# Optimization experiments

Measured on AMD Instinct MI355X. Metric: run time of the kernel, lower is better.

Reference implementation:

```python
import jax, jax.numpy as jnp
import numpy as np

SPATIAL_DECAY = 50.0
POS_SCALE = 1000.0  # spread positions so decay=50 gives realistic locality


def setup_inputs() -> dict:
    key = jax.random.key(0)
    k1, k2 = jax.random.split(key)
    N, D = 8192, 512
    features = jax.random.normal(k1, (N, D), dtype=jnp.float32)
    positions = jax.random.uniform(k2, (N, 2), dtype=jnp.float32) * POS_SCALE
    lambda_weight = jnp.asarray(0.5, dtype=jnp.float32)  # nn.Parameter init
    temperature = jnp.asarray(1.0, dtype=jnp.float32)    # nn.Parameter init
    return {"features": features, "positions": positions,
            "lambda_weight": lambda_weight, "temperature": temperature, "k": 20}


def reference(features, positions, lambda_weight, temperature, k):
    N = features.shape[0]
    # F.normalize(dim=1), eps=1e-12
    norms = jnp.linalg.norm(features, axis=1, keepdims=True)
    feat_norm = features / jnp.maximum(norms, 1e-12)
    sim = feat_norm @ feat_norm.T                                   # (N, N)
    # squared euclidean distances (cdist(p=2) then **2 == squared dist)
    sq = jnp.sum(positions * positions, axis=1)                      # (N,)
    d2 = jnp.maximum(sq[:, None] + sq[None, :] - 2.0 * (positions @ positions.T), 0.0)
    spatial = jnp.exp(-d2 / (2.0 * SPATIAL_DECAY ** 2))             # (N, N)
    lam = jax.nn.sigmoid(lambda_weight)
    adj = jax.nn.sigmoid((lam * sim + (1.0 - lam) * spatial) * temperature)
    # row-wise top-k mask, scatter 1.0 at top-k columns
    _, topk_idx = jax.lax.top_k(adj, k)                              # (N, k)
    rows = jnp.arange(N)[:, None]
    mask = jnp.zeros_like(adj).at[rows, topk_idx].set(1.0)
    return adj * mask, lam
```

## Files before the change

### kernel.cpp

```cpp
#include <hip/hip_runtime.h>
#include <hip/hip_fp16.h>
#include <math.h>

#define N 8192
#define D 512
#define KSEL 20
#define CAND_CAP 256
#define WINDOW 2.5e-3f
#define BS_EXTRA 6.2e-4f
#define ROWU 8192
#define FS_A 4096

typedef __attribute__((ext_vector_type(8))) short short8;
typedef __attribute__((ext_vector_type(4))) float f32x4;

__device__ __forceinline__ unsigned short f2bf(float x) {
  unsigned int u = __float_as_uint(x);
  unsigned int r = u + 0x7FFFu + ((u >> 16) & 1u);
  return (unsigned short)(r >> 16);
}

__device__ __forceinline__ unsigned int packh2(float a, float b) {
  return (unsigned int)__half_as_ushort(__float2half(a)) |
         ((unsigned int)__half_as_ushort(__float2half(b)) << 16);
}

__device__ __forceinline__ void gld16(const unsigned short* g, unsigned short* l) {
  __builtin_amdgcn_global_load_lds(
      (const __attribute__((address_space(1))) unsigned int*)g,
      (__attribute__((address_space(3))) unsigned int*)l, 16, 0, 0);
}

__device__ __forceinline__ int swz(int row, int cp) {
  return row * 64 + ((((cp >> 2) ^ (row & 15)) << 2) | (cp & 3));
}
__device__ __forceinline__ int swz4(int row, int q) {
  return row * 64 + ((q ^ (row & 15)) << 2);
}

__global__ __launch_bounds__(256) void prep_kernel(
    const float* __restrict__ feat, const float* __restrict__ pos,
    const float* __restrict__ lamw,
    float* __restrict__ normf, float* __restrict__ sqf,
    float* __restrict__ fn32, unsigned short* __restrict__ fnbf,
    float* __restrict__ out) {
  __shared__ float rowbuf[4][512];
  int w = threadIdx.x >> 6, lane = threadIdx.x & 63;
  float* rb = rowbuf[w];
  for (int i = 0; i < 8; i++) {
    int row = blockIdx.x * 32 + w * 8 + i;
    const float* f = feat + (size_t)row * D;
    float4 v0 = *(const float4*)(f + 4 * lane);
    float4 v1 = *(const float4*)(f + 256 + 4 * lane);
    *(float4*)&rb[4 * lane] = v0;
    *(float4*)&rb[256 + 4 * lane] = v1;
    __builtin_amdgcn_s_waitcnt(0);
    float s = 0.f;
    if (lane < 32) {
      int b = lane >> 3, j = lane & 7;
      const float* a = rb + b * 128 + j;
      float r = __fmul_rn(a[0], a[0]);
      #pragma unroll
      for (int k = 1; k < 16; k++)
        r = __fadd_rn(r, __fmul_rn(a[8 * k], a[8 * k]));
      r = __fadd_rn(r, __shfl_xor(r, 1, 64));
      r = __fadd_rn(r, __shfl_xor(r, 2, 64));
      r = __fadd_rn(r, __shfl_xor(r, 4, 64));
      r = __fadd_rn(r, __shfl_xor(r, 8, 64));
      r = __fadd_rn(r, __shfl_xor(r, 16, 64));
      s = r;
    }
    float st = __shfl(s, 0, 64);
    float nrm = fmaxf(__fsqrt_rn(st), 1e-12f);
    if (lane == 0) {
      normf[row] = nrm;
      float x = pos[2 * row], y = pos[2 * row + 1];
      sqf[row] = __fadd_rn(__fmul_rn(x, x), __fmul_rn(y, y));
      if (row == 0) {
        float e = (float)exp(-(double)lamw[0]);
        out[(size_t)N * N] = 1.0f / __fadd_rn(1.0f, e);
      }
    }
    float4 q0, q1;
    q0.x = v0.x / nrm; q0.y = v0.y / nrm; q0.z = v0.z / nrm; q0.w = v0.w / nrm;
    q1.x = v1.x / nrm; q1.y = v1.y / nrm; q1.z = v1.z / nrm; q1.w = v1.w / nrm;
    *(float4*)(fn32 + (size_t)row * D + 4 * lane) = q0;
    *(float4*)(fn32 + (size_t)row * D + 256 + 4 * lane) = q1;
    uint2 o0, o1;
    o0.x = (unsigned int)f2bf(q0.x) | ((unsigned int)f2bf(q0.y) << 16);
    o0.y = (unsigned int)f2bf(q0.z) | ((unsigned int)f2bf(q0.w) << 16);
    o1.x = (unsigned int)f2bf(q1.x) | ((unsigned int)f2bf(q1.y) << 16);
    o1.y = (unsigned int)f2bf(q1.z) | ((unsigned int)f2bf(q1.w) << 16);
    *(uint2*)(fnbf + (size_t)row * D + 4 * lane) = o0;
    *(uint2*)(fnbf + (size_t)row * D + 256 + 4 * lane) = o1;
  }
}

__global__ __launch_bounds__(256) void adj_kernel(
    const unsigned short* __restrict__ G,
    const float* __restrict__ pos, const float* __restrict__ sqf,
    const float* __restrict__ lamw, const float* __restrict__ temp,
    unsigned int* __restrict__ filt, int fs,
    unsigned int* __restrict__ out_u, int mode) {
  __shared__ __align__(16) unsigned char smem[32768];
  unsigned short* As = (unsigned short*)smem;
  unsigned short* Bs = As + 8192;
  unsigned int* tileT = (unsigned int*)smem;

  int L = blockIdx.x;
  int tid = threadIdx.x;

  if (L < 2048) {
    uint4 z = {0u, 0u, 0u, 0u};
    if (mode == 0) {
      size_t base = (size_t)L * 32768;
      #pragma unroll
      for (int it = 0; it < 32; it++)
        *(uint4*)(out_u + base + it * 1024 + tid * 4) = z;
    } else {
      #pragma unroll
      for (int it = 0; it < 16; it++) {
        int g = L * 16384 + it * 1024 + tid * 4;
        int r = g >> 12, c = g & 4095;
        *(uint4*)(out_u + (size_t)r * ROWU + 4096 + c) = z;
      }
    }
  }

  int by = (int)((129.0 - sqrt(129.0 * 129.0 - 8.0 * (double)L)) * 0.5);
  while (64 * (by + 1) - ((by + 1) * by) / 2 <= L) by++;
  while (64 * by - (by * (by - 1)) / 2 > L) by--;
  int bx = by + (L - (64 * by - (by * (by - 1)) / 2));

  int wave = tid >> 6, lane = tid & 63;
  int wr = (wave >> 1) * 64, wc = (wave & 1) * 64;
  int m = lane & 15, quad = lane >> 4;

  f32x4 acc[4][4];
  #pragma unroll
  for (int i = 0; i < 4; i++)
    #pragma unroll
    for (int j = 0; j < 4; j++) acc[i][j] = (f32x4){0.f, 0.f, 0.f, 0.f};

  for (int kt = 0; kt < D / 64; kt++) {
    #pragma unroll
    for (int i = 0; i < 4; i++) {
      int f = i * 256 + tid;
      int r = f >> 3, c = f & 7;
      int cs = (c + r) & 7;
      size_t goff = (size_t)r * D + kt * 64 + cs * 8;
      gld16(G + (size_t)(by * 128) * D + goff, &As[f * 8]);
      gld16(G + (size_t)(bx * 128) * D + goff, &Bs[f * 8]);
    }
    __syncthreads();
    #pragma unroll
    for (int h = 0; h < 2; h++) {
      short8 fa[4], fb[4];
      #pragma unroll
      for (int ti = 0; ti < 4; ti++) {
        int row = wr + ti * 16 + m;
        int cc = ((h * 4 + quad) - row) & 7;
        fa[ti] = *(const short8*)&As[row * 64 + cc * 8];
      }
      #pragma unroll
      for (int tj = 0; tj < 4; tj++) {
        int row = wc + tj * 16 + m;
        int cc = ((h * 4 + quad) - row) & 7;
        fb[tj] = *(const short8*)&Bs[row * 64 + cc * 8];
      }
      #pragma unroll
      for (int ti = 0; ti < 4; ti++)
        #pragma unroll
        for (int tj = 0; tj < 4; tj++)
          acc[ti][tj] = __builtin_amdgcn_mfma_f32_16x16x32_bf16(
              fa[ti], fb[tj], acc[ti][tj], 0, 0, 0);
    }
    __syncthreads();
  }

  float lam = 1.f / (1.f + __expf(-lamw[0]));
  float T = temp[0];
  float oml = 1.f - lam;
  bool offdiag = (bx != by);

  #pragma unroll
  for (int ti = 0; ti < 4; ti++) {
    int gi0 = by * 128 + wr + ti * 16 + quad * 4;
    float xi[4], yi[4], sqi[4];
    #pragma unroll
    for (int r = 0; r < 4; r++) {
      int gi = gi0 + r;
      xi[r] = pos[2 * gi]; yi[r] = pos[2 * gi + 1]; sqi[r] = sqf[gi];
    }
    #pragma unroll
    for (int tj = 0; tj < 4; tj++) {
      int gj = bx * 128 + wc + tj * 16 + m;
      float xj = pos[2 * gj], yj = pos[2 * gj + 1], sj = sqf[gj];
      f32x4 c = acc[ti][tj];
      float sv[4];
      #pragma unroll
      for (int r = 0; r < 4; r++) {
        float d2 = fmaxf(sqi[r] + sj - 2.f * (xi[r] * xj + yi[r] * yj), 0.f);
        float sp = __expf(-d2 * (1.f / 5000.f));
        sv[r] = (lam * c[r] + oml * sp) * T;
      }
      int cpL = (wc + tj * 16 + m) >> 1;
      #pragma unroll
      for (int r = 0; r < 4; r++) {
        float pv = __shfl_xor(sv[r], 1, 64);
        if (!(lane & 1)) {
          int rowL = wr + ti * 16 + quad * 4 + r;
          tileT[swz(rowL, cpL)] = packh2(sv[r], pv);
        }
      }
    }
  }
  __syncthreads();

  #pragma unroll
  for (int it = 0; it < 8; it++) {
    int idx4 = it * 256 + tid;
    int row = idx4 >> 4, q = idx4 & 15;
    uint4 v = *(uint4*)&tileT[swz4(row, q)];
    *(uint4*)(filt + (size_t)(by * 128 + row) * fs + bx * 64 + q * 4) = v;
  }

  if (offdiag) {
    #pragma unroll
    for (int it = 0; it < 8; it++) {
      int idx4 = it * 256 + tid;
      int c = idx4 >> 4, q = idx4 & 15;
      unsigned int wv[4];
      #pragma unroll
      for (int d = 0; d < 4; d++) {
        int p = q * 4 + d;
        unsigned int lo = tileT[swz(2 * p, c >> 1)];
        unsigned int hi = tileT[swz(2 * p + 1, c >> 1)];
        unsigned int h0 = (c & 1) ? (lo >> 16) : (lo & 0xFFFFu);
        unsigned int h1 = (c & 1) ? (hi >> 16) : (hi & 0xFFFFu);
        wv[d] = h0 | (h1 << 16);
      }
      uint4 v; v.x = wv[0]; v.y = wv[1]; v.z = wv[2]; v.w = wv[3];
      *(uint4*)(filt + (size_t)(bx * 128 + c) * fs + by * 64 + q * 4) = v;
    }
  }
}

__global__ __launch_bounds__(256, 4) void topk_kernel(
    const float* __restrict__ pos, const float* __restrict__ sqf,
    const float* __restrict__ lamw, const float* __restrict__ temp,
    const float* __restrict__ fn32,
    const unsigned int* __restrict__ filt, int fs,
    float* __restrict__ out, int doZero) {
  __shared__ float ai[D];
  __shared__ int   redi[2][4];
  __shared__ int   candIdx[CAND_CAP];
  __shared__ float candV[CAND_CAP];
  __shared__ int   selIdx[KSEL];
  __shared__ float selVal[KSEL];
  __shared__ int   cnt;

  int row = blockIdx.x, t = threadIdx.x;
  int lane = t & 63, wid = t >> 6;
  float* orow = out + (size_t)row * N;
  const uint4* fu4 = (const uint4*)(filt + (size_t)row * fs);
  const float* fn_i = fn32 + (size_t)row * D;

  float rv[32];
  #pragma unroll
  for (int q = 0; q < 4; q++) {
    uint4 u = fu4[t + 256 * q];
    unsigned int w[4] = {u.x, u.y, u.z, u.w};
    #pragma unroll
    for (int d = 0; d < 4; d++) {
      __half2 h2 = *reinterpret_cast<__half2*>(&w[d]);
      rv[8 * q + 2 * d]     = __low2float(h2);
      rv[8 * q + 2 * d + 1] = __high2float(h2);
    }
  }
  for (int k = t; k < D; k += 256) ai[k] = fn_i[k];
  if (t == 0) cnt = 0;
  __syncthreads();

  if (doZero) {
    float4 z4 = {0.f, 0.f, 0.f, 0.f};
    #pragma unroll
    for (int i = 0; i < 4; i++) *(float4*)&orow[4 * t + 1024 * i] = z4;
  }

  float lo = -1.0f, hi = 1.5f;
  for (int it = 0; it < 12; it++) {
    float mid = 0.5f * (lo + hi);
    int c = 0;
    #pragma unroll
    for (int q = 0; q < 32; q++) c += (rv[q] >= mid) ? 1 : 0;
    #pragma unroll
    for (int off = 32; off > 0; off >>= 1) c += __shfl_down(c, off, 64);
    if (lane == 0) redi[it & 1][wid] = c;
    __syncthreads();
    int tot = redi[it & 1][0] + redi[it & 1][1] + redi[it & 1][2] + redi[it & 1][3];
    if (tot >= KSEL) lo = mid; else hi = mid;
  }

  float thr = lo - (WINDOW + BS_EXTRA);
  #pragma unroll
  for (int q = 0; q < 32; q++) {
    if (rv[q] >= thr) {
      int p = atomicAdd(&cnt, 1);
      if (p < CAND_CAP) candIdx[p] = 8 * (t + 256 * (q >> 3)) + (q & 7);
    }
  }
  __syncthreads();
  int ncand = min(cnt, CAND_CAP);

  float lamf;
  { float e = (float)exp(-(double)lamw[0]); lamf = 1.0f / __fadd_rn(1.0f, e); }
  float omlf = __fadd_rn(1.0f, -lamf);
  float Tf = temp[0];
  float sq_i = sqf[row];
  float xi = pos[2 * row], yi = pos[2 * row + 1];

  if (t < ncand) {
    int j = candIdx[t];
    const float* fj = fn32 + (size_t)j * D;
    float accv = 0.0f;
    float4 buf[4], nxt[4];
    #pragma unroll
    for (int q = 0; q < 4; q++) buf[q] = *(const float4*)(fj + q * 4);
    for (int c16 = 0; c16 < 32; c16++) {
      if (c16 < 31) {
        #pragma unroll
        for (int q = 0; q < 4; q++)
          nxt[q] = *(const float4*)(fj + (c16 + 1) * 16 + q * 4);
      }
      #pragma unroll
      for (int q = 0; q < 4; q++) {
        float4 a4 = *(const float4*)&ai[c16 * 16 + q * 4];
        accv = __fmaf_rn(a4.x, buf[q].x, accv);
        accv = __fmaf_rn(a4.y, buf[q].y, accv);
        accv = __fmaf_rn(a4.z, buf[q].z, accv);
        accv = __fmaf_rn(a4.w, buf[q].w, accv);
      }
      #pragma unroll
      for (int q = 0; q < 4; q++) buf[q] = nxt[q];
    }
    float xj = pos[2 * j], yj = pos[2 * j + 1];
    float dot2 = __fmaf_rn(yi, yj, __fmul_rn(xi, xj));
    float Ssum = __fadd_rn(sq_i, sqf[j]);
    float d2 = fmaxf(__fadd_rn(Ssum, -__fmul_rn(2.0f, dot2)), 0.0f);
    float arg = (-d2) / 5000.0f;
    float sp = (float)exp((double)arg);
    float u = __fmul_rn(__fadd_rn(__fmul_rn(lamf, accv), __fmul_rn(omlf, sp)), Tf);
    float e = (float)exp(-(double)u);
    candV[t] = 1.0f / __fadd_rn(1.0f, e);
  }
  __syncthreads();

  if (t < 64) {
    for (int s = 0; s < KSEL; s++) {
      float bu = -1.0f; int bj = N, bs = 0;
      for (int c = t; c < ncand; c += 64) {
        float v = candV[c]; int j = candIdx[c];
        if (v > bu || (v == bu && j < bj)) { bu = v; bj = j; bs = c; }
      }
      #pragma unroll
      for (int off = 32; off > 0; off >>= 1) {
        float ov = __shfl_down(bu, off, 64);
        int   oj = __shfl_down(bj, off, 64);
        int   os = __shfl_down(bs, off, 64);
        if (ov > bu || (ov == bu && oj < bj)) { bu = ov; bj = oj; bs = os; }
      }
      if (t == 0) { selIdx[s] = bj; selVal[s] = bu; candV[bs] = -1.0f; }
      __builtin_amdgcn_s_waitcnt(0);
    }
  }
  __syncthreads();
  if (t < KSEL) orow[selIdx[t]] = selVal[t];
}

extern "C" void kernel_launch(void* const* d_in, const int* in_sizes, int n_in,
                              void* d_out, int out_size, void* d_ws, size_t ws_size,
                              hipStream_t stream) {
  const float* feat = (const float*)d_in[0];
  const float* pos  = (const float*)d_in[1];
  const float* lamw = (const float*)d_in[2];
  const float* temp = (const float*)d_in[3];
  float* out = (float*)d_out;
  unsigned int* out_u = (unsigned int*)d_out;

  float* normf = (float*)d_ws;
  float* sqf   = normf + N;
  float* fn32  = sqf + N;
  unsigned short* fnbf = (unsigned short*)(fn32 + (size_t)N * D);
  unsigned int* filtA = (unsigned int*)(fnbf + (size_t)N * D);
  size_t needA = (size_t)2 * N * 4 + (size_t)N * D * 4 + (size_t)N * D * 2 +
                 (size_t)N * FS_A * 4;

  prep_kernel<<<N / 32, 256, 0, stream>>>(feat, pos, lamw, normf, sqf,
                                          fn32, fnbf, out);
  if (ws_size >= needA) {
    adj_kernel<<<2080, 256, 0, stream>>>(fnbf, pos, sqf, lamw, temp,
                                         filtA, FS_A, out_u, 0);
    topk_kernel<<<N, 256, 0, stream>>>(pos, sqf, lamw, temp, fn32,
                                       filtA, FS_A, out, 0);
  } else {
    adj_kernel<<<2080, 256, 0, stream>>>(fnbf, pos, sqf, lamw, temp,
                                         out_u, ROWU, out_u, 1);
    topk_kernel<<<N, 256, 0, stream>>>(pos, sqf, lamw, temp, fn32,
                                       out_u, ROWU, out, 1);
  }
}
```

Measured before the change: 570.8 us.

## Process one row per wavefront in topk kernel with packed half2 threshold search

```diff
diff --git a/kernel.cpp b/kernel.cpp
--- a/kernel.cpp
+++ b/kernel.cpp
@@ -5,9 +5,7 @@
 #define N 8192
 #define D 512
 #define KSEL 20
-#define CAND_CAP 256
-#define WINDOW 2.5e-3f
-#define BS_EXTRA 6.2e-4f
+#define CAND_CAP 320
 #define ROWU 8192
 #define FS_A 4096
 
@@ -246,72 +244,88 @@
   }
 }
 
-__global__ __launch_bounds__(256, 4) void topk_kernel(
+__global__ __launch_bounds__(256) void topk_kernel(
     const float* __restrict__ pos, const float* __restrict__ sqf,
     const float* __restrict__ lamw, const float* __restrict__ temp,
     const float* __restrict__ fn32,
     const unsigned int* __restrict__ filt, int fs,
     float* __restrict__ out, int doZero) {
-  __shared__ float ai[D];
-  __shared__ int   redi[2][4];
-  __shared__ int   candIdx[CAND_CAP];
-  __shared__ float candV[CAND_CAP];
-  __shared__ int   selIdx[KSEL];
-  __shared__ float selVal[KSEL];
-  __shared__ int   cnt;
-
-  int row = blockIdx.x, t = threadIdx.x;
-  int lane = t & 63, wid = t >> 6;
+  __shared__ float ai[4][D];
+  __shared__ int   candIdx[4][CAND_CAP];
+  __shared__ float candV[4][CAND_CAP];
+  __shared__ int   selIdx[4][KSEL];
+  __shared__ float selVal[4][KSEL];
+  __shared__ int   cnt[4];
+
+  int w = threadIdx.x >> 6, lane = threadIdx.x & 63;
+  int row = blockIdx.x * 4 + w;
   float* orow = out + (size_t)row * N;
   const uint4* fu4 = (const uint4*)(filt + (size_t)row * fs);
   const float* fn_i = fn32 + (size_t)row * D;
 
-  float rv[32];
-  #pragma unroll
-  for (int q = 0; q < 4; q++) {
-    uint4 u = fu4[t + 256 * q];
-    unsigned int w[4] = {u.x, u.y, u.z, u.w};
-    #pragma unroll
-    for (int d = 0; d < 4; d++) {
-      __half2 h2 = *reinterpret_cast<__half2*>(&w[d]);
-      rv[8 * q + 2 * d]     = __low2float(h2);
-      rv[8 * q + 2 * d + 1] = __high2float(h2);
-    }
-  }
-  for (int k = t; k < D; k += 256) ai[k] = fn_i[k];
-  if (t == 0) cnt = 0;
-  __syncthreads();
-
-  if (doZero) {
-    float4 z4 = {0.f, 0.f, 0.f, 0.f};
-    #pragma unroll
-    for (int i = 0; i < 4; i++) *(float4*)&orow[4 * t + 1024 * i] = z4;
+  if (lane == 0) cnt[w] = 0;
+
+  unsigned int rv[64];
+  #pragma unroll
+  for (int q = 0; q < 16; q++) {
+    uint4 u = fu4[lane + 64 * q];
+    rv[4 * q] = u.x; rv[4 * q + 1] = u.y; rv[4 * q + 2] = u.z; rv[4 * q + 3] = u.w;
+  }
+  {
+    float4 a0 = *(const float4*)(fn_i + 4 * lane);
+    float4 a1 = *(const float4*)(fn_i + 256 + 4 * lane);
+    *(float4*)&ai[w][4 * lane] = a0;
+    *(float4*)&ai[w][256 + 4 * lane] = a1;
   }
 
   float lo = -1.0f, hi = 1.5f;
   for (int it = 0; it < 12; it++) {
     float mid = 0.5f * (lo + hi);
-    int c = 0;
-    #pragma unroll
-    for (int q = 0; q < 32; q++) c += (rv[q] >= mid) ? 1 : 0;
-    #pragma unroll
-    for (int off = 32; off > 0; off >>= 1) c += __shfl_down(c, off, 64);
-    if (lane == 0) redi[it & 1][wid] = c;
-    __syncthreads();
-    int tot = redi[it & 1][0] + redi[it & 1][1] + redi[it & 1][2] + redi[it & 1][3];
-    if (tot >= KSEL) lo = mid; else hi = mid;
-  }
-
-  float thr = lo - (WINDOW + BS_EXTRA);
-  #pragma unroll
-  for (int q = 0; q < 32; q++) {
-    if (rv[q] >= thr) {
-      int p = atomicAdd(&cnt, 1);
-      if (p < CAND_CAP) candIdx[p] = 8 * (t + 256 * (q >> 3)) + (q & 7);
-    }
-  }
-  __syncthreads();
-  int ncand = min(cnt, CAND_CAP);
+    __half2 m2 = __float2half2_rn(mid);
+    __half2 a2 = __float2half2_rn(0.f);
+    #pragma unroll
+    for (int r = 0; r < 64; r++) {
+      __half2 hv = *(__half2*)&rv[r];
+      a2 = __hadd2(a2, __hge2(hv, m2));
+    }
+    int c = (int)(__low2float(a2) + __high2float(a2));
+    #pragma unroll
+    for (int off = 32; off > 0; off >>= 1) c += __shfl_xor(c, off, 64);
+    if (c >= KSEL) lo = mid; else hi = mid;
+  }
+
+  float thr = lo - 3.7e-3f;
+  __half2 t2 = __float2half2_rn(thr - 6e-4f);
+  int myhits = 0;
+  #pragma unroll
+  for (int r = 0; r < 64; r++) {
+    __half2 hv = *(__half2*)&rv[r];
+    __half2 ge = __hge2(hv, t2);
+    unsigned int g = *(unsigned int*)&ge;
+    if (g) {
+      int j0 = 8 * lane + 512 * (r >> 2) + 2 * (r & 3);
+      if (g & 0xFFFFu) {
+        int p = atomicAdd(&cnt[w], 1);
+        if (p < CAND_CAP) candIdx[w][p] = j0;
+        myhits++;
+      }
+      if (g >> 16) {
+        int p = atomicAdd(&cnt[w], 1);
+        if (p < CAND_CAP) candIdx[w][p] = j0 + 1;
+        myhits++;
+      }
+    }
+  }
+  #pragma unroll
+  for (int off = 32; off > 0; off >>= 1) myhits += __shfl_xor(myhits, off, 64);
+  int ncand = min(myhits, CAND_CAP);
+  __builtin_amdgcn_s_waitcnt(0);
+
+  if (doZero) {
+    float4 z4 = {0.f, 0.f, 0.f, 0.f};
+    #pragma unroll
+    for (int i = 0; i < 16; i++) *(float4*)&orow[4 * lane + 256 * i] = z4;
+  }
 
   float lamf;
   { float e = (float)exp(-(double)lamw[0]); lamf = 1.0f / __fadd_rn(1.0f, e); }
@@ -320,8 +334,8 @@
   float sq_i = sqf[row];
   float xi = pos[2 * row], yi = pos[2 * row + 1];
 
-  if (t < ncand) {
-    int j = candIdx[t];
+  for (int ci = lane; ci < ncand; ci += 64) {
+    int j = candIdx[w][ci];
     const float* fj = fn32 + (size_t)j * D;
     float accv = 0.0f;
     float4 buf[4], nxt[4];
@@ -335,7 +349,7 @@
       }
       #pragma unroll
       for (int q = 0; q < 4; q++) {
-        float4 a4 = *(const float4*)&ai[c16 * 16 + q * 4];
+        float4 a4 = *(const float4*)&ai[w][c16 * 16 + q * 4];
         accv = __fmaf_rn(a4.x, buf[q].x, accv);
         accv = __fmaf_rn(a4.y, buf[q].y, accv);
         accv = __fmaf_rn(a4.z, buf[q].z, accv);
@@ -352,30 +366,29 @@
     float sp = (float)exp((double)arg);
     float u = __fmul_rn(__fadd_rn(__fmul_rn(lamf, accv), __fmul_rn(omlf, sp)), Tf);
     float e = (float)exp(-(double)u);
-    candV[t] = 1.0f / __fadd_rn(1.0f, e);
-  }
-  __syncthreads();
-
-  if (t < 64) {
-    for (int s = 0; s < KSEL; s++) {
-      float bu = -1.0f; int bj = N, bs = 0;
-      for (int c = t; c < ncand; c += 64) {
-        float v = candV[c]; int j = candIdx[c];
-        if (v > bu || (v == bu && j < bj)) { bu = v; bj = j; bs = c; }
-      }
-      #pragma unroll
-      for (int off = 32; off > 0; off >>= 1) {
-        float ov = __shfl_down(bu, off, 64);
-        int   oj = __shfl_down(bj, off, 64);
-        int   os = __shfl_down(bs, off, 64);
-        if (ov > bu || (ov == bu && oj < bj)) { bu = ov; bj = oj; bs = os; }
-      }
-      if (t == 0) { selIdx[s] = bj; selVal[s] = bu; candV[bs] = -1.0f; }
-      __builtin_amdgcn_s_waitcnt(0);
-    }
-  }
-  __syncthreads();
-  if (t < KSEL) orow[selIdx[t]] = selVal[t];
+    candV[w][ci] = 1.0f / __fadd_rn(1.0f, e);
+  }
+  __builtin_amdgcn_s_waitcnt(0);
+
+  for (int s = 0; s < KSEL; s++) {
+    float bu = -1.0f; int bj = N, bs = 0;
+    for (int c = lane; c < ncand; c += 64) {
+      float v = candV[w][c]; int j = candIdx[w][c];
+      if (v > bu || (v == bu && j < bj)) { bu = v; bj = j; bs = c; }
+    }
+    #pragma unroll
+    for (int off = 32; off > 0; off >>= 1) {
+      float ov = __shfl_down(bu, off, 64);
+      int   oj = __shfl_down(bj, off, 64);
+      int   os = __shfl_down(bs, off, 64);
+      if (ov > bu || (ov == bu && oj < bj)) { bu = ov; bj = oj; bs = os; }
+    }
+    if (lane == 0) { selIdx[w][s] = bj; selVal[w][s] = bu; candV[w][bs] = -1.0f; }
+    __builtin_amdgcn_s_waitcnt(0);
+  }
+
+  __builtin_amdgcn_s_waitcnt(0);
+  if (lane < KSEL) orow[selIdx[w][lane]] = selVal[w][lane];
 }
 
 extern "C" void kernel_launch(void* const* d_in, const int* in_sizes, int n_in,
@@ -401,12 +414,12 @@
   if (ws_size >= needA) {
     adj_kernel<<<2080, 256, 0, stream>>>(fnbf, pos, sqf, lamw, temp,
                                          filtA, FS_A, out_u, 0);
-    topk_kernel<<<N, 256, 0, stream>>>(pos, sqf, lamw, temp, fn32,
-                                       filtA, FS_A, out, 0);
+    topk_kernel<<<N / 4, 256, 0, stream>>>(pos, sqf, lamw, temp, fn32,
+                                           filtA, FS_A, out, 0);
   } else {
     adj_kernel<<<2080, 256, 0, stream>>>(fnbf, pos, sqf, lamw, temp,
                                          out_u, ROWU, out_u, 1);
-    topk_kernel<<<N, 256, 0, stream>>>(pos, sqf, lamw, temp, fn32,
-                                       out_u, ROWU, out, 1);
-  }
-}
+    topk_kernel<<<N / 4, 256, 0, stream>>>(pos, sqf, lamw, temp, fn32,
+                                           out_u, ROWU, out, 1);
+  }
+}
```

Result: slower. 853.0 us (+49.4%).

## Interleave output zeroing with GEMM loads and use packed half2 threshold counting

Applied to the files above, without the earlier changes.

```diff
diff --git a/kernel.cpp b/kernel.cpp
--- a/kernel.cpp
+++ b/kernel.cpp
@@ -5,9 +5,7 @@
 #define N 8192
 #define D 512
 #define KSEL 20
-#define CAND_CAP 256
-#define WINDOW 2.5e-3f
-#define BS_EXTRA 6.2e-4f
+#define CAND_CAP 320
 #define ROWU 8192
 #define FS_A 4096
 
@@ -110,23 +108,6 @@
   int L = blockIdx.x;
   int tid = threadIdx.x;
 
-  if (L < 2048) {
-    uint4 z = {0u, 0u, 0u, 0u};
-    if (mode == 0) {
-      size_t base = (size_t)L * 32768;
-      #pragma unroll
-      for (int it = 0; it < 32; it++)
-        *(uint4*)(out_u + base + it * 1024 + tid * 4) = z;
-    } else {
-      #pragma unroll
-      for (int it = 0; it < 16; it++) {
-        int g = L * 16384 + it * 1024 + tid * 4;
-        int r = g >> 12, c = g & 4095;
-        *(uint4*)(out_u + (size_t)r * ROWU + 4096 + c) = z;
-      }
-    }
-  }
-
   int by = (int)((129.0 - sqrt(129.0 * 129.0 - 8.0 * (double)L)) * 0.5);
   while (64 * (by + 1) - ((by + 1) * by) / 2 <= L) by++;
   while (64 * by - (by * (by - 1)) / 2 > L) by--;
@@ -151,6 +132,22 @@
       size_t goff = (size_t)r * D + kt * 64 + cs * 8;
       gld16(G + (size_t)(by * 128) * D + goff, &As[f * 8]);
       gld16(G + (size_t)(bx * 128) * D + goff, &Bs[f * 8]);
+    }
+    if (L < 2048) {
+      uint4 z = {0u, 0u, 0u, 0u};
+      if (mode == 0) {
+        size_t base = (size_t)L * 32768 + (size_t)kt * 4096;
+        #pragma unroll
+        for (int it2 = 0; it2 < 4; it2++)
+          *(uint4*)(out_u + base + it2 * 1024 + tid * 4) = z;
+      } else {
+        #pragma unroll
+        for (int it2 = 0; it2 < 2; it2++) {
+          int g = L * 16384 + (kt * 2 + it2) * 1024 + tid * 4;
+          int r = g >> 12, c = g & 4095;
+          *(uint4*)(out_u + (size_t)r * ROWU + 4096 + c) = z;
+        }
+      }
     }
     __syncthreads();
     #pragma unroll
@@ -266,17 +263,11 @@
   const uint4* fu4 = (const uint4*)(filt + (size_t)row * fs);
   const float* fn_i = fn32 + (size_t)row * D;
 
-  float rv[32];
+  unsigned int rv[16];
   #pragma unroll
   for (int q = 0; q < 4; q++) {
     uint4 u = fu4[t + 256 * q];
-    unsigned int w[4] = {u.x, u.y, u.z, u.w};
-    #pragma unroll
-    for (int d = 0; d < 4; d++) {
-      __half2 h2 = *reinterpret_cast<__half2*>(&w[d]);
-      rv[8 * q + 2 * d]     = __low2float(h2);
-      rv[8 * q + 2 * d + 1] = __high2float(h2);
-    }
+    rv[4 * q] = u.x; rv[4 * q + 1] = u.y; rv[4 * q + 2] = u.z; rv[4 * q + 3] = u.w;
   }
   for (int k = t; k < D; k += 256) ai[k] = fn_i[k];
   if (t == 0) cnt = 0;
@@ -291,9 +282,12 @@
   float lo = -1.0f, hi = 1.5f;
   for (int it = 0; it < 12; it++) {
     float mid = 0.5f * (lo + hi);
-    int c = 0;
-    #pragma unroll
-    for (int q = 0; q < 32; q++) c += (rv[q] >= mid) ? 1 : 0;
+    __half2 m2 = __float2half2_rn(mid);
+    __half2 a2 = __float2half2_rn(0.f);
+    #pragma unroll
+    for (int r = 0; r < 16; r++)
+      a2 = __hadd2(a2, __hge2(*(__half2*)&rv[r], m2));
+    int c = (int)(__low2float(a2) + __high2float(a2));
     #pragma unroll
     for (int off = 32; off > 0; off >>= 1) c += __shfl_down(c, off, 64);
     if (lane == 0) redi[it & 1][wid] = c;
@@ -302,12 +296,21 @@
     if (tot >= KSEL) lo = mid; else hi = mid;
   }
 
-  float thr = lo - (WINDOW + BS_EXTRA);
+  __half2 t2 = __float2half2_rn(lo - 3.7e-3f - 6e-4f);
   #pragma unroll
-  for (int q = 0; q < 32; q++) {
-    if (rv[q] >= thr) {
-      int p = atomicAdd(&cnt, 1);
-      if (p < CAND_CAP) candIdx[p] = 8 * (t + 256 * (q >> 3)) + (q & 7);
+  for (int r = 0; r < 16; r++) {
+    __half2 ge = __hge2(*(__half2*)&rv[r], t2);
+    unsigned int g = *(unsigned int*)&ge;
+    if (g) {
+      int j0 = 8 * (t + 256 * (r >> 2)) + 2 * (r & 3);
+      if (g & 0xFFFFu) {
+        int p = atomicAdd(&cnt, 1);
+        if (p < CAND_CAP) candIdx[p] = j0;
+      }
+      if (g >> 16) {
+        int p = atomicAdd(&cnt, 1);
+        if (p < CAND_CAP) candIdx[p] = j0 + 1;
+      }
     }
   }
   __syncthreads();
```

New measurement: 560.4 us. About the same (-1.8%).
